# Kernel optimization log

Measured on AMD Instinct MI355X. Metric: run time of the kernel, lower is better.

Reference implementation:

```python
import jax, jax.numpy as jnp
import numpy as np
import math

B, S, HID = 2, 2048, 1024
D = 64            # size_per_head
H = HID // D      # num heads = 16
ROT = 32          # rotary_hsize = size_per_head // 2


def _apply_rotary(qk, sinusoids):
    # qk: [B, S, H, D]; sinusoids: [B, 2, S, ROT]
    sin = sinusoids[:, 0, :, None, :]   # [B, S, 1, ROT]
    cos = sinusoids[:, 1, :, None, :]
    qk_rope = qk[..., :ROT]
    # torch.stack([-a[..., ::2], a[..., 1::2]], -1).reshape(a.shape)
    rot2 = jnp.stack([-qk_rope[..., ::2], qk_rope[..., 1::2]], axis=-1).reshape(qk_rope.shape)
    qk_rope = qk_rope * cos + rot2 * sin
    return jnp.concatenate([qk_rope, qk[..., ROT:]], axis=-1)


def setup_inputs() -> dict:
    key = jax.random.key(0)
    ks = jax.random.split(key, 8)
    sc = 1.0 / math.sqrt(HID)
    return {
        "x": jax.random.normal(ks[0], (B, S, HID), jnp.float32),
        "sinusoids": jax.random.normal(ks[1], (B, 2, S, ROT), jnp.float32),
        "attention_bias": jax.random.uniform(ks[2], (B, 1, S, S), jnp.float32),
        "Wq": jax.random.normal(ks[3], (HID, HID), jnp.float32) * sc,
        "bq": jnp.zeros((HID,), jnp.float32),
        "Wk": jax.random.normal(ks[4], (HID, HID), jnp.float32) * sc,
        "bk": jnp.zeros((HID,), jnp.float32),
        "Wv": jax.random.normal(ks[5], (HID, HID), jnp.float32) * sc,
        "bv": jnp.zeros((HID,), jnp.float32),
        "Wo": jax.random.normal(ks[6], (HID, HID), jnp.float32) * sc,
    }


def reference(x, sinusoids, attention_bias, Wq, bq, Wk, bk, Wv, bv, Wo):
    q = (x @ Wq + bq).reshape(B, S, H, D)
    k = (x @ Wk + bk).reshape(B, S, H, D)
    v = (x @ Wv + bv).reshape(B, S, H, D)
    # original concatenates q,k along the heads dim before rotary; since rotary
    # broadcasts over heads, applying it to each separately is identical math
    q = _apply_rotary(q, sinusoids)
    k = _apply_rotary(k, sinusoids)
    q = q / math.sqrt(D)
    scores = jnp.einsum('bqhd,bkhd->bhqk', q, k)          # [B,H,S,S]
    probs = jax.nn.softmax(scores, axis=-1)
    probs = probs * attention_bias                         # multiplicative bias AFTER softmax
    out = jnp.einsum('bhqk,bkhd->bqhd', probs, v)          # [B,S,H,D]
    out = out.reshape(B, S, HID)
    return out @ Wo
```

## Files before the change

kernel.cpp:

```cpp
#include <hip/hip_runtime.h>
#include <hip/hip_bf16.h>
#include <math.h>

#define B_   2
#define S_   2048
#define HID_ 1024
#define D_   64
#define H_   16
#define ROT_ 32
#define M_   (B_*S_)

typedef __attribute__((ext_vector_type(8))) short  short8;
typedef __attribute__((ext_vector_type(4))) float  floatx4;

__device__ __forceinline__ float bf2f(unsigned short u) {
  unsigned int x = ((unsigned int)u) << 16;
  return __builtin_bit_cast(float, x);
}
__device__ __forceinline__ unsigned short f2bf(float f) {
  unsigned int x = __builtin_bit_cast(unsigned int, f);
  x += 0x7fffu + ((x >> 16) & 1u);
  return (unsigned short)(x >> 16);
}
__device__ __forceinline__ float exp2a(float x) {
  float r; asm volatile("v_exp_f32 %0, %1\n\ts_nop 0" : "=v"(r) : "v"(x)); return r;
}
__device__ __forceinline__ float rcpa(float x) {
  float r; asm volatile("v_rcp_f32 %0, %1\n\ts_nop 0" : "=v"(r) : "v"(x)); return r;
}
__device__ __forceinline__ void gload_lds16(const unsigned short* g, unsigned short* l) {
  __builtin_amdgcn_global_load_lds(
      (const __attribute__((address_space(1))) unsigned int*)g,
      (__attribute__((address_space(3))) unsigned int*)l, 16, 0, 0);
}

__global__ void cast_bf16(const float* __restrict__ in, unsigned short* __restrict__ out) {
  int i = (blockIdx.x * 256 + threadIdx.x) * 4;
  floatx4 v = *(const floatx4*)(in + i);
  unsigned short o[4];
  o[0] = f2bf(v[0]); o[1] = f2bf(v[1]); o[2] = f2bf(v[2]); o[3] = f2bf(v[3]);
  *(unsigned long long*)(out + i) = *(unsigned long long*)o;
}

__global__ void transW(const float* __restrict__ W0, const float* __restrict__ W1,
                       const float* __restrict__ W2, const float* __restrict__ W3,
                       unsigned short* __restrict__ T0, unsigned short* __restrict__ T1,
                       unsigned short* __restrict__ T2, unsigned short* __restrict__ T3) {
  const float* W; unsigned short* T;
  int z = blockIdx.z;
  if (z == 0)      { W = W0; T = T0; }
  else if (z == 1) { W = W1; T = T1; }
  else if (z == 2) { W = W2; T = T2; }
  else             { W = W3; T = T3; }
  __shared__ float tile[32][33];
  int bx = blockIdx.x * 32, by = blockIdx.y * 32;
  int tx = threadIdx.x, ty = threadIdx.y;
  #pragma unroll
  for (int j = 0; j < 4; j++)
    tile[ty + j*8][tx] = W[(size_t)(by + ty + j*8) * HID_ + bx + tx];
  __syncthreads();
  #pragma unroll
  for (int j = 0; j < 4; j++)
    T[(size_t)(bx + ty + j*8) * HID_ + by + tx] = f2bf(tile[tx][ty + j*8]);
}

template <int MODE>
__global__ __launch_bounds__(256) void gemm_bt(
    const unsigned short* __restrict__ A,
    const unsigned short* __restrict__ Bt0, const unsigned short* __restrict__ Bt1,
    const unsigned short* __restrict__ Bt2,
    const float* __restrict__ bias0, const float* __restrict__ bias1,
    const float* __restrict__ bias2,
    void* __restrict__ out0, void* __restrict__ out1, void* __restrict__ out2,
    const float* __restrict__ sins, float sc0)
{
  const unsigned short* Bt; const float* bias; void* Out; float sc;
  if (blockIdx.z == 0)      { Bt = Bt0; bias = bias0; Out = out0; sc = sc0; }
  else if (blockIdx.z == 1) { Bt = Bt1; bias = bias1; Out = out1; sc = 1.f; }
  else                      { Bt = Bt2; bias = bias2; Out = out2; sc = 1.f; }
  const int K = HID_, N = HID_;
  int m0 = blockIdx.y * 128, n0 = blockIdx.x * 128;
  __shared__ alignas(16) unsigned short sA[128 * 32];
  __shared__ alignas(16) unsigned short sB[128 * 32];
  int t = threadIdx.x;
  int lane = t & 63, wave = t >> 6;
  int quad = lane >> 4, l16 = lane & 15;
  int wr = wave >> 1, wc = wave & 1;

  int srow = (lane >> 2), scol = (lane & 3) * 8;
  const unsigned short* gA0 = A  + (size_t)(m0 + wave*32 +  0 + srow) * K + scol;
  const unsigned short* gA1 = A  + (size_t)(m0 + wave*32 + 16 + srow) * K + scol;
  const unsigned short* gB0 = Bt + (size_t)(n0 + wave*32 +  0 + srow) * K + scol;
  const unsigned short* gB1 = Bt + (size_t)(n0 + wave*32 + 16 + srow) * K + scol;
  unsigned short* lA0 = sA + (wave*32 +  0) * 32;
  unsigned short* lA1 = sA + (wave*32 + 16) * 32;
  unsigned short* lB0 = sB + (wave*32 +  0) * 32;
  unsigned short* lB1 = sB + (wave*32 + 16) * 32;

  floatx4 acc[4][4];
  #pragma unroll
  for (int i = 0; i < 4; i++)
    #pragma unroll
    for (int j = 0; j < 4; j++)
      acc[i][j] = (floatx4){0.f, 0.f, 0.f, 0.f};

  for (int k0 = 0; k0 < K; k0 += 32) {
    gload_lds16(gA0 + k0, lA0);
    gload_lds16(gA1 + k0, lA1);
    gload_lds16(gB0 + k0, lB0);
    gload_lds16(gB1 + k0, lB1);
    __syncthreads();
    short8 af[4], bf[4];
    #pragma unroll
    for (int i = 0; i < 4; i++) {
      af[i] = *(const short8*)(sA + (wr * 64 + i * 16 + l16) * 32 + quad * 8);
      bf[i] = *(const short8*)(sB + (wc * 64 + i * 16 + l16) * 32 + quad * 8);
    }
    #pragma unroll
    for (int i = 0; i < 4; i++)
      #pragma unroll
      for (int j = 0; j < 4; j++)
        acc[i][j] = __builtin_amdgcn_mfma_f32_16x16x32_bf16(af[i], bf[j], acc[i][j], 0, 0, 0);
    __syncthreads();
  }

  #pragma unroll
  for (int i = 0; i < 4; i++) {
    int mbase = m0 + wr * 64 + i * 16 + quad * 4;
    #pragma unroll
    for (int j = 0; j < 4; j++) {
      int n = n0 + wc * 64 + j * 16 + l16;
      float bv = bias ? bias[n] : 0.f;
      if (MODE == 1) {
        #pragma unroll
        for (int r = 0; r < 4; r++)
          ((float*)Out)[(size_t)(mbase + r) * N + n] = acc[i][j][r] + bv;
      } else if (blockIdx.z == 2) {
        int bb = mbase >> 11, ss = mbase & 2047;
        int hh = n >> 6, dd = n & 63;
        unsigned short pk[4];
        #pragma unroll
        for (int r = 0; r < 4; r++) pk[r] = f2bf(acc[i][j][r] + bv);
        *(unsigned long long*)((unsigned short*)Out +
            (((size_t)(bb * H_ + hh) * D_ + dd) * S_ + ss)) = *(unsigned long long*)pk;
      } else if (j < 2) {
        int jh = j * 16 + l16;
        #pragma unroll
        for (int r = 0; r < 4; r++) {
          int row = mbase + r, bb = row >> 11, ss = row & 2047;
          float sn = sins[((size_t)(bb * 2 + 0) * S_ + ss) * ROT_ + jh];
          float cs = sins[((size_t)(bb * 2 + 1) * S_ + ss) * ROT_ + jh];
          float f = (jh & 1) ? (cs + sn) : (cs - sn);
          ((unsigned short*)Out)[(size_t)row * N + n] = f2bf((acc[i][j][r] + bv) * f * sc);
        }
      } else {
        #pragma unroll
        for (int r = 0; r < 4; r++)
          ((unsigned short*)Out)[(size_t)(mbase + r) * N + n] = f2bf((acc[i][j][r] + bv) * sc);
      }
    }
  }
}

__global__ __launch_bounds__(256) void attn(
    const unsigned short* __restrict__ Q, const unsigned short* __restrict__ Kb,
    const unsigned short* __restrict__ Vt, const float* __restrict__ bias,
    unsigned short* __restrict__ Out)
{
  int b = blockIdx.z, h = blockIdx.y, q0 = blockIdx.x * 64;
  int t = threadIdx.x;
  int lane = t & 63, wave = t >> 6;
  int quad = lane >> 4, l16 = lane & 15;
  const int RS = H_ * D_;

  __shared__ alignas(16) unsigned short sK[2][64 * 72];
  __shared__ alignas(16) unsigned short sV[2][64 * 72];
  __shared__ alignas(16) unsigned short sP[4][16 * 72];

  const unsigned short* Qbase = Q + ((size_t)(b * S_) * H_ + h) * D_;
  const unsigned short* Kbase = Kb + ((size_t)(b * S_) * H_ + h) * D_;
  const unsigned short* Vbase = Vt + ((size_t)(b * H_) + h) * D_ * S_;

  int qrow = q0 + wave * 16 + l16;
  short8 qf[2];
  qf[0] = *(const short8*)(Qbase + (size_t)qrow * RS + quad * 8);
  qf[1] = *(const short8*)(Qbase + (size_t)qrow * RS + 32 + quad * 8);

  int kr0 = t >> 3, dg = t & 7;
  int kr1 = kr0 + 32;

  const float* bptr[4];
  #pragma unroll
  for (int r = 0; r < 4; r++)
    bptr[r] = bias + (size_t)b * S_ * S_ + (size_t)(q0 + wave * 16 + quad * 4 + r) * S_;

  float l_run[4] = {0.f, 0.f, 0.f, 0.f};
  floatx4 accO[4];
  #pragma unroll
  for (int d = 0; d < 4; d++) accO[d] = (floatx4){0.f, 0.f, 0.f, 0.f};

  floatx4 kpre[2], vpre[2];
  kpre[0] = *(const floatx4*)(Kbase + (size_t)kr0 * RS + dg * 8);
  kpre[1] = *(const floatx4*)(Kbase + (size_t)kr1 * RS + dg * 8);
  vpre[0] = *(const floatx4*)(Vbase + (size_t)kr0 * S_ + dg * 8);
  vpre[1] = *(const floatx4*)(Vbase + (size_t)kr1 * S_ + dg * 8);
  *(floatx4*)(&sK[0][kr0 * 72 + dg * 8]) = kpre[0];
  *(floatx4*)(&sK[0][kr1 * 72 + dg * 8]) = kpre[1];
  *(floatx4*)(&sV[0][kr0 * 72 + dg * 8]) = vpre[0];
  *(floatx4*)(&sV[0][kr1 * 72 + dg * 8]) = vpre[1];
  kpre[0] = *(const floatx4*)(Kbase + (size_t)(64 + kr0) * RS + dg * 8);
  kpre[1] = *(const floatx4*)(Kbase + (size_t)(64 + kr1) * RS + dg * 8);
  vpre[0] = *(const floatx4*)(Vbase + (size_t)kr0 * S_ + 64 + dg * 8);
  vpre[1] = *(const floatx4*)(Vbase + (size_t)kr1 * S_ + 64 + dg * 8);

  for (int it = 0; it < S_ / 64; ++it) {
    int cur = it & 1, nxt = cur ^ 1;
    int k0 = it * 64;
    __syncthreads();

    if (it < S_ / 64 - 1) {
      *(floatx4*)(&sK[nxt][kr0 * 72 + dg * 8]) = kpre[0];
      *(floatx4*)(&sK[nxt][kr1 * 72 + dg * 8]) = kpre[1];
      *(floatx4*)(&sV[nxt][kr0 * 72 + dg * 8]) = vpre[0];
      *(floatx4*)(&sV[nxt][kr1 * 72 + dg * 8]) = vpre[1];
    }
    {
      int k0n = ((it + 2) & (S_ / 64 - 1)) * 64;
      kpre[0] = *(const floatx4*)(Kbase + (size_t)(k0n + kr0) * RS + dg * 8);
      kpre[1] = *(const floatx4*)(Kbase + (size_t)(k0n + kr1) * RS + dg * 8);
      vpre[0] = *(const floatx4*)(Vbase + (size_t)kr0 * S_ + k0n + dg * 8);
      vpre[1] = *(const floatx4*)(Vbase + (size_t)kr1 * S_ + k0n + dg * 8);
    }

    floatx4 sreg[4];
    #pragma unroll
    for (int ks = 0; ks < 4; ks++) {
      short8 kf0 = *(const short8*)(&sK[cur][(ks * 16 + l16) * 72 + quad * 8]);
      short8 kf1 = *(const short8*)(&sK[cur][(ks * 16 + l16) * 72 + 32 + quad * 8]);
      floatx4 s = (floatx4){0.f, 0.f, 0.f, 0.f};
      s = __builtin_amdgcn_mfma_f32_16x16x32_bf16(qf[0], kf0, s, 0, 0, 0);
      s = __builtin_amdgcn_mfma_f32_16x16x32_bf16(qf[1], kf1, s, 0, 0, 0);
      sreg[ks] = s;
    }

    #pragma unroll
    for (int ks = 0; ks < 4; ks++)
      #pragma unroll
      for (int r = 0; r < 4; r++) {
        float p = exp2a(sreg[ks][r]);
        sreg[ks][r] = p;
        l_run[r] += p;
      }

    #pragma unroll
    for (int ks = 0; ks < 4; ks++)
      #pragma unroll
      for (int r = 0; r < 4; r++) {
        float pb = sreg[ks][r] * bptr[r][k0 + ks * 16 + l16];
        sP[wave][(quad * 4 + r) * 72 + ks * 16 + l16] = f2bf(pb);
      }
    short8 pf0 = *(const short8*)(&sP[wave][l16 * 72 + quad * 8]);
    short8 pf1 = *(const short8*)(&sP[wave][l16 * 72 + 32 + quad * 8]);
    #pragma unroll
    for (int d = 0; d < 4; d++) {
      short8 vf0 = *(const short8*)(&sV[cur][(d * 16 + l16) * 72 + quad * 8]);
      short8 vf1 = *(const short8*)(&sV[cur][(d * 16 + l16) * 72 + 32 + quad * 8]);
      accO[d] = __builtin_amdgcn_mfma_f32_16x16x32_bf16(pf0, vf0, accO[d], 0, 0, 0);
      accO[d] = __builtin_amdgcn_mfma_f32_16x16x32_bf16(pf1, vf1, accO[d], 0, 0, 0);
    }
  }

  #pragma unroll
  for (int r = 0; r < 4; r++) {
    float v = l_run[r];
    v += __shfl_xor(v, 1);
    v += __shfl_xor(v, 2);
    v += __shfl_xor(v, 4);
    v += __shfl_xor(v, 8);
    l_run[r] = rcpa(v);
  }
  #pragma unroll
  for (int d = 0; d < 4; d++)
    #pragma unroll
    for (int r = 0; r < 4; r++) {
      int qq = q0 + wave * 16 + quad * 4 + r;
      int dd = d * 16 + l16;
      Out[((size_t)(b * S_ + qq) * H_ + h) * D_ + dd] = f2bf(accO[d][r] * l_run[r]);
    }
}

extern "C" void kernel_launch(void* const* d_in, const int* in_sizes, int n_in,
                              void* d_out, int out_size, void* d_ws, size_t ws_size,
                              hipStream_t stream) {
  (void)in_sizes; (void)n_in; (void)out_size; (void)ws_size;
  const float* x    = (const float*)d_in[0];
  const float* sins = (const float*)d_in[1];
  const float* ab   = (const float*)d_in[2];
  const float* Wq   = (const float*)d_in[3];
  const float* bq   = (const float*)d_in[4];
  const float* Wk   = (const float*)d_in[5];
  const float* bk   = (const float*)d_in[6];
  const float* Wv   = (const float*)d_in[7];
  const float* bv   = (const float*)d_in[8];
  const float* Wo   = (const float*)d_in[9];
  float* out = (float*)d_out;
  char* ws = (char*)d_ws;

  unsigned short* xb  = (unsigned short*)(ws);
  unsigned short* Wqt = (unsigned short*)(ws + ((size_t) 8 << 20));
  unsigned short* Wkt = (unsigned short*)(ws + ((size_t)10 << 20));
  unsigned short* Wvt = (unsigned short*)(ws + ((size_t)12 << 20));
  unsigned short* Wot = (unsigned short*)(ws + ((size_t)14 << 20));
  unsigned short* Qb  = (unsigned short*)(ws + ((size_t)16 << 20));
  unsigned short* Kb  = (unsigned short*)(ws + ((size_t)24 << 20));
  unsigned short* Vtb = (unsigned short*)(ws + ((size_t)32 << 20));
  unsigned short* Ab  = (unsigned short*)(ws + ((size_t)40 << 20));

  const float c1 = 0.125f * 1.44269504088896f;

  cast_bf16<<<dim3((M_ * HID_) / (256 * 4)), dim3(256), 0, stream>>>(x, xb);
  transW<<<dim3(32, 32, 4), dim3(32, 8), 0, stream>>>(Wq, Wk, Wv, Wo, Wqt, Wkt, Wvt, Wot);
  gemm_bt<0><<<dim3(8, 32, 3), dim3(256), 0, stream>>>(xb, Wqt, Wkt, Wvt, bq, bk, bv,
                                                       Qb, Kb, Vtb, sins, c1);
  attn<<<dim3(S_ / 64, H_, B_), dim3(256), 0, stream>>>(Qb, Kb, Vtb, ab, Ab);
  gemm_bt<1><<<dim3(8, 32, 1), dim3(256), 0, stream>>>(Ab, Wot, Wot, Wot,
                                                       nullptr, nullptr, nullptr,
                                                       out, out, out, sins, 1.f);
}
```

Before: 290.9 us.

## Restructure attention to 32x32 MFMA with register-resident P and 128-row blocks

Rewrites the attention kernel so each wave handles 32 query rows using 32x32 MFMA tiles. It computes S^T (K as the A operand) so the softmax probabilities land directly in the B-operand layout for the PV MFMA. This removes the per-wave shared-memory round trip for P. Bias is loaded as vectorized float4 reads instead of scalar gathers, and each block now covers 128 queries, halving the grid and reusing each K/V tile across twice as many rows. In exchange, register pressure rises with two 16-float accumulators, and occupancy may drop with fewer blocks.

```diff
diff --git a/kernel.cpp b/kernel.cpp
--- a/kernel.cpp
+++ b/kernel.cpp
@@ -10,8 +10,10 @@
 #define ROT_ 32
 #define M_   (B_*S_)
 
+typedef __attribute__((ext_vector_type(4))) short  short4v;
 typedef __attribute__((ext_vector_type(8))) short  short8;
 typedef __attribute__((ext_vector_type(4))) float  floatx4;
+typedef __attribute__((ext_vector_type(16))) float floatx16;
 
 __device__ __forceinline__ float bf2f(unsigned short u) {
   unsigned int x = ((unsigned int)u) << 16;
@@ -167,51 +169,52 @@
     const unsigned short* __restrict__ Vt, const float* __restrict__ bias,
     unsigned short* __restrict__ Out)
 {
-  int b = blockIdx.z, h = blockIdx.y, q0 = blockIdx.x * 64;
+  int b = blockIdx.z, h = blockIdx.y;
   int t = threadIdx.x;
   int lane = t & 63, wave = t >> 6;
-  int quad = lane >> 4, l16 = lane & 15;
+  int l32 = lane & 31, hl = lane >> 5;
+  int q0 = blockIdx.x * 128 + wave * 32;
   const int RS = H_ * D_;
 
   __shared__ alignas(16) unsigned short sK[2][64 * 72];
   __shared__ alignas(16) unsigned short sV[2][64 * 72];
-  __shared__ alignas(16) unsigned short sP[4][16 * 72];
 
   const unsigned short* Qbase = Q + ((size_t)(b * S_) * H_ + h) * D_;
   const unsigned short* Kbase = Kb + ((size_t)(b * S_) * H_ + h) * D_;
   const unsigned short* Vbase = Vt + ((size_t)(b * H_) + h) * D_ * S_;
 
-  int qrow = q0 + wave * 16 + l16;
-  short8 qf[2];
-  qf[0] = *(const short8*)(Qbase + (size_t)qrow * RS + quad * 8);
-  qf[1] = *(const short8*)(Qbase + (size_t)qrow * RS + 32 + quad * 8);
-
-  int kr0 = t >> 3, dg = t & 7;
-  int kr1 = kr0 + 32;
-
-  const float* bptr[4];
-  #pragma unroll
-  for (int r = 0; r < 4; r++)
-    bptr[r] = bias + (size_t)b * S_ * S_ + (size_t)(q0 + wave * 16 + quad * 4 + r) * S_;
-
-  float l_run[4] = {0.f, 0.f, 0.f, 0.f};
-  floatx4 accO[4];
-  #pragma unroll
-  for (int d = 0; d < 4; d++) accO[d] = (floatx4){0.f, 0.f, 0.f, 0.f};
-
-  floatx4 kpre[2], vpre[2];
-  kpre[0] = *(const floatx4*)(Kbase + (size_t)kr0 * RS + dg * 8);
-  kpre[1] = *(const floatx4*)(Kbase + (size_t)kr1 * RS + dg * 8);
-  vpre[0] = *(const floatx4*)(Vbase + (size_t)kr0 * S_ + dg * 8);
-  vpre[1] = *(const floatx4*)(Vbase + (size_t)kr1 * S_ + dg * 8);
-  *(floatx4*)(&sK[0][kr0 * 72 + dg * 8]) = kpre[0];
-  *(floatx4*)(&sK[0][kr1 * 72 + dg * 8]) = kpre[1];
-  *(floatx4*)(&sV[0][kr0 * 72 + dg * 8]) = vpre[0];
-  *(floatx4*)(&sV[0][kr1 * 72 + dg * 8]) = vpre[1];
-  kpre[0] = *(const floatx4*)(Kbase + (size_t)(64 + kr0) * RS + dg * 8);
-  kpre[1] = *(const floatx4*)(Kbase + (size_t)(64 + kr1) * RS + dg * 8);
-  vpre[0] = *(const floatx4*)(Vbase + (size_t)kr0 * S_ + 64 + dg * 8);
-  vpre[1] = *(const floatx4*)(Vbase + (size_t)kr1 * S_ + 64 + dg * 8);
+  short8 qf[4];
+  {
+    const unsigned short* qp = Qbase + (size_t)(q0 + l32) * RS + 8 * hl;
+    qf[0] = *(const short8*)(qp);
+    qf[1] = *(const short8*)(qp + 16);
+    qf[2] = *(const short8*)(qp + 32);
+    qf[3] = *(const short8*)(qp + 48);
+  }
+
+  int srow = t >> 2, sq = t & 3;
+  const unsigned short* gK = Kbase + (size_t)srow * RS + sq * 16;
+  const unsigned short* gV = Vbase + (size_t)srow * S_ + sq * 16;
+  const int wOff = srow * 72 + sq * 16;
+
+  const float* bp = bias + (size_t)b * S_ * S_ + (size_t)(q0 + l32) * S_ + 4 * hl;
+
+  float l_run = 0.f;
+  floatx16 o0, o1;
+  #pragma unroll
+  for (int r = 0; r < 16; r++) { o0[r] = 0.f; o1[r] = 0.f; }
+
+  floatx4 kp[2], vp[2];
+  kp[0] = *(const floatx4*)(gK);     kp[1] = *(const floatx4*)(gK + 8);
+  vp[0] = *(const floatx4*)(gV);     vp[1] = *(const floatx4*)(gV + 8);
+  *(floatx4*)(&sK[0][wOff])     = kp[0];
+  *(floatx4*)(&sK[0][wOff + 8]) = kp[1];
+  *(floatx4*)(&sV[0][wOff])     = vp[0];
+  *(floatx4*)(&sV[0][wOff + 8]) = vp[1];
+  kp[0] = *(const floatx4*)(gK + (size_t)64 * RS);
+  kp[1] = *(const floatx4*)(gK + (size_t)64 * RS + 8);
+  vp[0] = *(const floatx4*)(gV + 64);
+  vp[1] = *(const floatx4*)(gV + 64 + 8);
 
   for (int it = 0; it < S_ / 64; ++it) {
     int cur = it & 1, nxt = cur ^ 1;
@@ -219,74 +222,77 @@
     __syncthreads();
 
     if (it < S_ / 64 - 1) {
-      *(floatx4*)(&sK[nxt][kr0 * 72 + dg * 8]) = kpre[0];
-      *(floatx4*)(&sK[nxt][kr1 * 72 + dg * 8]) = kpre[1];
-      *(floatx4*)(&sV[nxt][kr0 * 72 + dg * 8]) = vpre[0];
-      *(floatx4*)(&sV[nxt][kr1 * 72 + dg * 8]) = vpre[1];
+      *(floatx4*)(&sK[nxt][wOff])     = kp[0];
+      *(floatx4*)(&sK[nxt][wOff + 8]) = kp[1];
+      *(floatx4*)(&sV[nxt][wOff])     = vp[0];
+      *(floatx4*)(&sV[nxt][wOff + 8]) = vp[1];
     }
     {
-      int k0n = ((it + 2) & (S_ / 64 - 1)) * 64;
-      kpre[0] = *(const floatx4*)(Kbase + (size_t)(k0n + kr0) * RS + dg * 8);
-      kpre[1] = *(const floatx4*)(Kbase + (size_t)(k0n + kr1) * RS + dg * 8);
-      vpre[0] = *(const floatx4*)(Vbase + (size_t)kr0 * S_ + k0n + dg * 8);
-      vpre[1] = *(const floatx4*)(Vbase + (size_t)kr1 * S_ + k0n + dg * 8);
-    }
-
-    floatx4 sreg[4];
-    #pragma unroll
-    for (int ks = 0; ks < 4; ks++) {
-      short8 kf0 = *(const short8*)(&sK[cur][(ks * 16 + l16) * 72 + quad * 8]);
-      short8 kf1 = *(const short8*)(&sK[cur][(ks * 16 + l16) * 72 + 32 + quad * 8]);
-      floatx4 s = (floatx4){0.f, 0.f, 0.f, 0.f};
-      s = __builtin_amdgcn_mfma_f32_16x16x32_bf16(qf[0], kf0, s, 0, 0, 0);
-      s = __builtin_amdgcn_mfma_f32_16x16x32_bf16(qf[1], kf1, s, 0, 0, 0);
-      sreg[ks] = s;
-    }
-
-    #pragma unroll
-    for (int ks = 0; ks < 4; ks++)
-      #pragma unroll
-      for (int r = 0; r < 4; r++) {
-        float p = exp2a(sreg[ks][r]);
-        sreg[ks][r] = p;
-        l_run[r] += p;
+      int k2 = ((it + 2) & (S_ / 64 - 1)) * 64;
+      kp[0] = *(const floatx4*)(gK + (size_t)k2 * RS);
+      kp[1] = *(const floatx4*)(gK + (size_t)k2 * RS + 8);
+      vp[0] = *(const floatx4*)(gV + k2);
+      vp[1] = *(const floatx4*)(gV + k2 + 8);
+    }
+
+    floatx4 bl[8];
+    #pragma unroll
+    for (int cc = 0; cc < 2; cc++)
+      #pragma unroll
+      for (int rg = 0; rg < 4; rg++)
+        bl[cc * 4 + rg] = *(const floatx4*)(bp + k0 + cc * 32 + 8 * rg);
+
+    floatx16 st[2];
+    #pragma unroll
+    for (int cc = 0; cc < 2; cc++) {
+      floatx16 s;
+      #pragma unroll
+      for (int r = 0; r < 16; r++) s[r] = 0.f;
+      #pragma unroll
+      for (int ks = 0; ks < 4; ks++) {
+        short8 kf = *(const short8*)(&sK[cur][(cc * 32 + l32) * 72 + 16 * ks + 8 * hl]);
+        s = __builtin_amdgcn_mfma_f32_32x32x16_bf16(kf, qf[ks], s, 0, 0, 0);
       }
-
-    #pragma unroll
-    for (int ks = 0; ks < 4; ks++)
-      #pragma unroll
-      for (int r = 0; r < 4; r++) {
-        float pb = sreg[ks][r] * bptr[r][k0 + ks * 16 + l16];
-        sP[wave][(quad * 4 + r) * 72 + ks * 16 + l16] = f2bf(pb);
+      st[cc] = s;
+    }
+
+    short4v pf[2][4];
+    #pragma unroll
+    for (int cc = 0; cc < 2; cc++)
+      #pragma unroll
+      for (int rg = 0; rg < 4; rg++) {
+        short4v pk;
+        #pragma unroll
+        for (int j = 0; j < 4; j++) {
+          float p = exp2a(st[cc][rg * 4 + j]);
+          l_run += p;
+          pk[j] = (short)f2bf(p * bl[cc * 4 + rg][j]);
+        }
+        pf[cc][rg] = pk;
       }
-    short8 pf0 = *(const short8*)(&sP[wave][l16 * 72 + quad * 8]);
-    short8 pf1 = *(const short8*)(&sP[wave][l16 * 72 + 32 + quad * 8]);
-    #pragma unroll
-    for (int d = 0; d < 4; d++) {
-      short8 vf0 = *(const short8*)(&sV[cur][(d * 16 + l16) * 72 + quad * 8]);
-      short8 vf1 = *(const short8*)(&sV[cur][(d * 16 + l16) * 72 + 32 + quad * 8]);
-      accO[d] = __builtin_amdgcn_mfma_f32_16x16x32_bf16(pf0, vf0, accO[d], 0, 0, 0);
-      accO[d] = __builtin_amdgcn_mfma_f32_16x16x32_bf16(pf1, vf1, accO[d], 0, 0, 0);
-    }
-  }
-
-  #pragma unroll
-  for (int r = 0; r < 4; r++) {
-    float v = l_run[r];
-    v += __shfl_xor(v, 1);
-    v += __shfl_xor(v, 2);
-    v += __shfl_xor(v, 4);
-    v += __shfl_xor(v, 8);
-    l_run[r] = rcpa(v);
-  }
-  #pragma unroll
-  for (int d = 0; d < 4; d++)
-    #pragma unroll
-    for (int r = 0; r < 4; r++) {
-      int qq = q0 + wave * 16 + quad * 4 + r;
-      int dd = d * 16 + l16;
-      Out[((size_t)(b * S_ + qq) * H_ + h) * D_ + dd] = f2bf(accO[d][r] * l_run[r]);
-    }
+
+    #pragma unroll
+    for (int cc = 0; cc < 2; cc++)
+      #pragma unroll
+      for (int g = 0; g < 4; g++) {
+        int kcol = cc * 32 + 8 * g + 4 * hl;
+        short4v vf0 = *(const short4v*)(&sV[cur][(l32)      * 72 + kcol]);
+        short4v vf1 = *(const short4v*)(&sV[cur][(32 + l32) * 72 + kcol]);
+        o0 = __builtin_amdgcn_mfma_f32_32x32x8bf16_1k(pf[cc][g], vf0, o0, 0, 0, 0);
+        o1 = __builtin_amdgcn_mfma_f32_32x32x8bf16_1k(pf[cc][g], vf1, o1, 0, 0, 0);
+      }
+  }
+
+  float linv = rcpa(l_run + __shfl_xor(l_run, 32));
+
+  #pragma unroll
+  for (int r = 0; r < 16; r++) {
+    int q_local = (r & 3) + 8 * (r >> 2) + 4 * hl;
+    float sc = __shfl(linv, q_local);
+    size_t base = ((size_t)(b * S_ + q0 + q_local) * H_ + h) * D_;
+    Out[base + l32]      = f2bf(o0[r] * sc);
+    Out[base + 32 + l32] = f2bf(o1[r] * sc);
+  }
 }
 
 extern "C" void kernel_launch(void* const* d_in, const int* in_sizes, int n_in,
@@ -322,7 +328,7 @@
   transW<<<dim3(32, 32, 4), dim3(32, 8), 0, stream>>>(Wq, Wk, Wv, Wo, Wqt, Wkt, Wvt, Wot);
   gemm_bt<0><<<dim3(8, 32, 3), dim3(256), 0, stream>>>(xb, Wqt, Wkt, Wvt, bq, bk, bv,
                                                        Qb, Kb, Vtb, sins, c1);
-  attn<<<dim3(S_ / 64, H_, B_), dim3(256), 0, stream>>>(Qb, Kb, Vtb, ab, Ab);
+  attn<<<dim3(S_ / 128, H_, B_), dim3(256), 0, stream>>>(Qb, Kb, Vtb, ab, Ab);
   gemm_bt<1><<<dim3(8, 32, 1), dim3(256), 0, stream>>>(Ab, Wot, Wot, Wot,
                                                        nullptr, nullptr, nullptr,
                                                        out, out, out, sins, 1.f);
```

New measurement: 278.0 us. 4.4% less time.
